# Kernel optimization log

Hardware: AMD Instinct MI355X
Metric: run time of the kernel (lower is better)

Reference implementation:

```python
import jax, jax.numpy as jnp
import numpy as np

N_NODES = 50000
N_EDGES = 1600000
IN_DIM = 128
HID = 64
EPS = 1e-6


def setup_inputs() -> dict:
    key = jax.random.key(0)
    ks = jax.random.split(key, 12)
    def g(k, shape, scale):
        return jax.random.normal(k, shape, dtype=jnp.float32) * scale
    x = g(ks[0], (N_NODES, IN_DIM), 1.0)
    edge_index = jax.random.randint(ks[1], (2, N_EDGES), 0, N_NODES, dtype=jnp.int64)
    return {
        "x": x,
        "edge_index": edge_index,
        "w0s": g(ks[2], (IN_DIM, HID), 1.0 / np.sqrt(IN_DIM)),
        "w0n": g(ks[3], (IN_DIM, HID), 1.0 / np.sqrt(IN_DIM)),
        "w1s": g(ks[4], (HID, HID), 1.0 / np.sqrt(HID)),
        "w1n": g(ks[5], (HID, HID), 1.0 / np.sqrt(HID)),
        "w2s": g(ks[6], (HID, HID), 1.0 / np.sqrt(HID)),
        "w2n": g(ks[7], (HID, HID), 1.0 / np.sqrt(HID)),
        "mw1": g(ks[8], (HID, 32), 1.0 / np.sqrt(HID)),
        "mb1": jnp.zeros((32,), jnp.float32),
        "mw2": g(ks[9], (32, 1), 1.0 / np.sqrt(32.0)),
        "mb2": jnp.zeros((1,), jnp.float32),
    }


def _uhg_layer(h, src, dst, inv_deg, ws, wn):
    # transform-then-gather (cheaper: GEMM at node granularity, gather at edge granularity)
    msg = (h @ wn)[src]                                    # [E, HID]
    agg = jax.ops.segment_sum(msg, dst, num_segments=N_NODES) * inv_deg  # mean over in-neighbors
    h2 = jax.nn.relu(h @ ws + agg)
    # projective (UHG) normalization: map embedding back onto the unit sphere / projective rep
    return h2 / (jnp.linalg.norm(h2, axis=-1, keepdims=True) + EPS)


def reference(x, edge_index, w0s, w0n, w1s, w1n, w2s, w2n, mw1, mb1, mw2, mb2):
    src, dst = edge_index[0], edge_index[1]
    deg = jax.ops.segment_sum(jnp.ones((N_EDGES,), jnp.float32), dst, num_segments=N_NODES)
    inv_deg = (1.0 / jnp.maximum(deg, 1.0))[:, None]       # [N,1]
    h = _uhg_layer(x, src, dst, inv_deg, w0s, w0n)
    h = _uhg_layer(h, src, dst, inv_deg, w1s, w1n)
    h = _uhg_layer(h, src, dst, inv_deg, w2s, w2n)
    h = jax.nn.relu(h @ mw1 + mb1)                         # [N,32]
    return jax.nn.sigmoid(h @ mw2 + mb2)                   # [N,1]
```

## Files before the change

### kernel.cpp

```cpp
#include <hip/hip_runtime.h>
#include <hip/hip_bf16.h>
#include <math.h>

#define N_NODES 50000
#define N_EDGES 1600000
#define IN_DIM  128
#define HID     64
#define EPB     4096
#define NBLK    391
#define NB      391
#define CAP     8192
#define PBKT    8192
#define GEMM0G  782
static constexpr float EPS = 1e-6f;

typedef __attribute__((ext_vector_type(8))) short          short8;
typedef __attribute__((ext_vector_type(4))) int            i32x4;
typedef __attribute__((ext_vector_type(4))) float          f32x4;
typedef __attribute__((ext_vector_type(2))) float          f32x2;

__device__ __forceinline__ unsigned short f2bf(float f) {
    union { float f; unsigned int i; } c; c.f = f;
    unsigned int r = c.i + 0x7FFFu + ((c.i >> 16) & 1u);
    return (unsigned short)(r >> 16);
}
__device__ __forceinline__ unsigned char f2fp8(float f) {
    int p = __builtin_amdgcn_cvt_pk_fp8_f32(f, f, 0, false);
    return (unsigned char)(p & 0xff);
}


template <int K>
__device__ __forceinline__ void pack_body(const float* __restrict__ wS,
                                          const float* __restrict__ wN,
                                          unsigned short* __restrict__ pS,
                                          unsigned short* __restrict__ pN, int blk) {
    constexpr int NSLOT = (K / 32) * 4 * 64;
    int slot = blk * 256 + (int)threadIdx.x;
    if (slot >= NSLOT) return;
    int lane = slot & 63;
    int ct   = slot >> 6;
    int t    = ct & 3;
    int c    = ct >> 2;
    int m    = lane & 15;
    int quad = lane >> 4;
    int col  = t * 16 + m;
#pragma unroll
    for (int j = 0; j < 8; ++j) {
        int k = c * 32 + quad * 8 + j;
        pS[slot * 8 + j] = f2bf(wS[k * 64 + col]);
        pN[slot * 8 + j] = f2bf(wN[k * 64 + col]);
    }
}

template <int K, bool F32IN>
__device__ __forceinline__ void gemm_body(
    const void* __restrict__ Av,
    const unsigned short* __restrict__ pS,
    const unsigned short* __restrict__ pN,
    float* __restrict__ hs, unsigned char* __restrict__ hnq, int blk) {
    constexpr int NC = K / 32;
    int lane = threadIdx.x & 63;
    int wv   = threadIdx.x >> 6;
    int tile = blk * 4 + wv;
    if (tile >= N_NODES / 16) return;
    int m    = lane & 15;
    int quad = lane >> 4;

    const short8* pSf = (const short8*)pS;
    const short8* pNf = (const short8*)pN;

    f32x4 accS[4], accN[4];
#pragma unroll
    for (int t = 0; t < 4; ++t) {
        accS[t] = (f32x4){0.f, 0.f, 0.f, 0.f};
        accN[t] = (f32x4){0.f, 0.f, 0.f, 0.f};
    }
#pragma unroll
    for (int c = 0; c < NC; ++c) {
        short8 a;
        if constexpr (F32IN) {
            const float* Af = (const float*)Av + ((size_t)tile * 16 + m) * K + quad * 8 + c * 32;
            f32x4 a0 = *(const f32x4*)Af;
            f32x4 a1 = *(const f32x4*)(Af + 4);
#pragma unroll
            for (int k = 0; k < 4; ++k) a[k]     = (short)f2bf(a0[k]);
#pragma unroll
            for (int k = 0; k < 4; ++k) a[k + 4] = (short)f2bf(a1[k]);
        } else {
            const short8* Af = (const short8*)((const unsigned short*)Av +
                               ((size_t)tile * 16 + m) * K + quad * 8);
            a = Af[c * 4];
        }
#pragma unroll
        for (int t = 0; t < 4; ++t) {
            short8 bs = pSf[(c * 4 + t) * 64 + lane];
            short8 bn = pNf[(c * 4 + t) * 64 + lane];
            accS[t] = __builtin_amdgcn_mfma_f32_16x16x32_bf16(a, bs, accS[t], 0, 0, 0);
            accN[t] = __builtin_amdgcn_mfma_f32_16x16x32_bf16(a, bn, accN[t], 0, 0, 0);
        }
    }
    int row0 = tile * 16 + quad * 4;
#pragma unroll
    for (int t = 0; t < 4; ++t) {
#pragma unroll
        for (int r = 0; r < 4; ++r) {
            size_t o = (size_t)(row0 + r) * HID + t * 16 + m;
            hs[o]  = accS[t][r];
            hnq[o] = f2fp8(accN[t][r]);
        }
    }
}

__global__ __launch_bounds__(256) void bucket_count_pack(
    const int* __restrict__ ei, int* __restrict__ bc,
    const float* __restrict__ w0s, const float* __restrict__ w0n,
    const float* __restrict__ w1s, const float* __restrict__ w1n,
    const float* __restrict__ w2s, const float* __restrict__ w2n,
    unsigned short* __restrict__ p0S, unsigned short* __restrict__ p0N,
    unsigned short* __restrict__ p1S, unsigned short* __restrict__ p1N,
    unsigned short* __restrict__ p2S, unsigned short* __restrict__ p2N,
    unsigned char* __restrict__ hnqA, unsigned char* __restrict__ hnqB,
    int* __restrict__ gcount) {
    if (blockIdx.x >= NBLK) {
        int blk = blockIdx.x - NBLK;
        if (blk == 7) {
            if (threadIdx.x >= 128 && threadIdx.x < 144)
                ((unsigned int*)(hnqA + (size_t)N_NODES * HID))[threadIdx.x - 128] = 0u;
            if (threadIdx.x >= 144 && threadIdx.x < 160)
                ((unsigned int*)(hnqB + (size_t)N_NODES * HID))[threadIdx.x - 144] = 0u;
            if (threadIdx.x == 160) gcount[0] = 0;
        }
        if (blk < 4)      pack_body<IN_DIM>(w0s, w0n, p0S, p0N, blk);
        else if (blk < 6) pack_body<HID>(w1s, w1n, p1S, p1N, blk - 4);
        else              pack_body<HID>(w2s, w2n, p2S, p2N, blk - 6);
        return;
    }
    __shared__ int hist[NB];
    for (int i = threadIdx.x; i < NB; i += 256) hist[i] = 0;
    __syncthreads();
    int base = blockIdx.x * EPB;
    int lim  = min(EPB, N_EDGES - base);
    for (int i = threadIdx.x; i < lim; i += 256)
        atomicAdd(&hist[ei[N_EDGES + base + i] >> 7], 1);
    __syncthreads();
    for (int b = threadIdx.x; b < NB; b += 256)
        bc[blockIdx.x * NB + b] = hist[b];
}

__global__ __launch_bounds__(256) void col_sumfix_gemm0(
    int* __restrict__ bc, int* __restrict__ bucketBase, int* __restrict__ bucketTot,
    int* __restrict__ gcount,
    const float* __restrict__ x,
    const unsigned short* __restrict__ p0S, const unsigned short* __restrict__ p0N,
    float* __restrict__ hs, unsigned char* __restrict__ hnq) {
    if (blockIdx.x >= NB) {
        gemm_body<IN_DIM, true>(x, p0S, p0N, hs, hnq, blockIdx.x - NB);
        return;
    }
    __shared__ int vals[NBLK];
    int b = blockIdx.x;
    for (int i = threadIdx.x; i < NBLK; i += 256) vals[i] = bc[i * NB + b];
    __syncthreads();
    if (threadIdx.x < 64) {
        int lane = threadIdx.x;
        int s = 0;
        for (int i = lane; i < NBLK; i += 64) s += vals[i];
#pragma unroll
        for (int off = 32; off >= 1; off >>= 1) s += __shfl_xor(s, off, 64);
        int base = 0;
        if (lane == 0) {
            base = atomicAdd(gcount, s);
            bucketBase[b] = base;
            bucketTot[b]  = s;
        }
        base = __shfl(base, 0, 64);
        int carry = base;
        for (int bs = 0; bs < NBLK; bs += 64) {
            int i = bs + lane;
            int v = (i < NBLK) ? vals[i] : 0;
            int incl = v;
#pragma unroll
            for (int off = 1; off < 64; off <<= 1) {
                int t = __shfl_up(incl, off, 64);
                if (lane >= off) incl += t;
            }
            if (i < NBLK) vals[i] = carry + incl - v;
            carry += __shfl(incl, 63, 64);
        }
    }
    __syncthreads();
    for (int i = threadIdx.x; i < NBLK; i += 256) bc[i * NB + b] = vals[i];
}

__global__ __launch_bounds__(256) void bucket_scatter(const int* __restrict__ ei,
                                                      const int* __restrict__ bc,
                                                      unsigned int* __restrict__ bucketPacked) {
    __shared__ int cur[NB];
    for (int b = threadIdx.x; b < NB; b += 256)
        cur[b] = bc[blockIdx.x * NB + b];
    __syncthreads();
    int base = blockIdx.x * EPB;
    int lim  = min(EPB, N_EDGES - base);
    for (int i = threadIdx.x; i < lim; i += 256) {
        int s = ei[base + i];
        int d = ei[N_EDGES + base + i];
        int pos = atomicAdd(&cur[d >> 7], 1);
        bucketPacked[pos] = ((unsigned int)s << 7) | (unsigned int)(d & 127);
    }
}

__global__ __launch_bounds__(256) void node_scan_scatter_pad(
    const unsigned int* __restrict__ bucketPacked,
    const int* __restrict__ bucketBase, const int* __restrict__ bucketTot,
    int* __restrict__ pbeg, int* __restrict__ rdeg, int* __restrict__ csr_pad) {
    __shared__ int cnt[128];
    __shared__ int half0;
    __shared__ unsigned int stage[CAP];
    int tid = threadIdx.x;
    if (tid < 128) cnt[tid] = 0;
    __syncthreads();
    int beg = bucketBase[blockIdx.x];
    int n   = bucketTot[blockIdx.x];
    for (int i = tid; i < n; i += 256) {
        unsigned int e = bucketPacked[beg + i];
        if (i < CAP) stage[i] = e;
        atomicAdd(&cnt[e & 127], 1);
    }
    __syncthreads();
    int lane = tid & 63;
    int v    = (tid < 128) ? cnt[tid] : 0;
    int vp   = (v + 7) & ~7;
    int incl = vp;
#pragma unroll
    for (int off = 1; off < 64; off <<= 1) {
        int t = __shfl_up(incl, off, 64);
        if (lane >= off) incl += t;
    }
    if (tid == 63) half0 = incl;
    __syncthreads();
    int start = blockIdx.x * PBKT + ((tid >= 64 && tid < 128) ? half0 : 0) + incl - vp;
    int node  = blockIdx.x * 128 + tid;
    if (tid < 128 && node < N_NODES) {
        pbeg[node] = start;
        rdeg[node] = v;
        for (int j = v; j < vp; ++j) csr_pad[start + j] = N_NODES;
        cnt[tid] = start;
    }
    __syncthreads();
    for (int i = tid; i < n; i += 256) {
        unsigned int e = (i < CAP) ? stage[i] : bucketPacked[beg + i];
        int pos = atomicAdd(&cnt[e & 127], 1);
        csr_pad[pos] = (int)(e >> 7);
    }
}

template <bool MLP>
__global__ __launch_bounds__(256) void agg_update(
    const int* __restrict__ pbeg, const int* __restrict__ rdeg,
    const int* __restrict__ csr_pad,
    const unsigned char* __restrict__ hnq, const float* __restrict__ hs,
    const unsigned short* __restrict__ pS, const unsigned short* __restrict__ pN,
    float* __restrict__ hs2, unsigned char* __restrict__ hnq2,
    const float* __restrict__ mw1, const float* __restrict__ mb1,
    const float* __restrict__ mw2, const float* __restrict__ mb2,
    float* __restrict__ out) {
    __shared__ unsigned short sA[MLP ? 1 : 16 * 80];
    __shared__ float sW1[MLP ? HID * 32 : 1];
    __shared__ float sW2[MLP ? 32 : 1];
    __shared__ float sB1[MLP ? 32 : 1];
    __shared__ float sH[MLP ? 16 * 68 : 1];
    if (MLP) {
        for (int i = threadIdx.x; i < HID * 32; i += 256) sW1[i] = mw1[i];
        if (threadIdx.x < 32) { sW2[threadIdx.x] = mw2[threadIdx.x]; sB1[threadIdx.x] = mb1[threadIdx.x]; }
        __syncthreads();
    }
    int sn   = threadIdx.x >> 4;
    int r    = threadIdx.x & 15;
    int node = blockIdx.x * 16 + sn;
    int beg  = pbeg[node];
    int dg   = rdeg[node];
    f32x4 h  = *(const f32x4*)(hs + (size_t)node * HID + r * 4);
    int nbat = (dg + 7) >> 3;
    const i32x4* ip = (const i32x4*)(csr_pad + beg);
    unsigned r4 = (unsigned)(r * 4);

    f32x2 acc2[2];
    acc2[0] = (f32x2){0.f, 0.f};
    acc2[1] = (f32x2){0.f, 0.f};

#pragma unroll 2
    for (int t = 0; t < nbat; ++t) {
        i32x4 a = ip[2 * t];
        i32x4 b = ip[2 * t + 1];
        unsigned wv[8];
#pragma unroll
        for (int u = 0; u < 4; ++u)
            wv[u]     = *(const unsigned*)(hnq + (((unsigned)a[u] << 6) + r4));
#pragma unroll
        for (int u = 0; u < 4; ++u)
            wv[u + 4] = *(const unsigned*)(hnq + (((unsigned)b[u] << 6) + r4));
#pragma unroll
        for (int u = 0; u < 8; ++u) {
#if __has_builtin(__builtin_amdgcn_cvt_pk_f32_fp8)
            acc2[0] += __builtin_amdgcn_cvt_pk_f32_fp8((int)wv[u], false);
            acc2[1] += __builtin_amdgcn_cvt_pk_f32_fp8((int)wv[u], true);
#else
            acc2[0] += (f32x2){__builtin_amdgcn_cvt_f32_fp8((int)wv[u], 0),
                               __builtin_amdgcn_cvt_f32_fp8((int)wv[u], 1)};
            acc2[1] += (f32x2){__builtin_amdgcn_cvt_f32_fp8((int)wv[u], 2),
                               __builtin_amdgcn_cvt_f32_fp8((int)wv[u], 3)};
#endif
        }
    }

    float acc[4] = {acc2[0][0], acc2[0][1], acc2[1][0], acc2[1][1]};
    float invdeg = 1.0f / fmaxf((float)dg, 1.0f);
    float v[4], ss = 0.f;
#pragma unroll
    for (int k = 0; k < 4; ++k) {
        v[k] = fmaxf(fmaf(acc[k], invdeg, h[k]), 0.f);
        ss += v[k] * v[k];
    }
    ss += __shfl_xor(ss, 1, 64);
    ss += __shfl_xor(ss, 2, 64);
    ss += __shfl_xor(ss, 4, 64);
    ss += __shfl_xor(ss, 8, 64);
    float rs = 1.0f / (sqrtf(ss) + EPS);

    if constexpr (!MLP) {
        unsigned short* ap = &sA[sn * 80 + r * 4];
#pragma unroll
        for (int k = 0; k < 4; ++k) ap[k] = f2bf(v[k] * rs);
        __syncthreads();
        int lane = threadIdx.x & 63;
        int wv_  = threadIdx.x >> 6;
        int m    = lane & 15;
        int quad = lane >> 4;
        const short8* pB = (const short8*)((wv_ < 2) ? pS : pN);
        int t0 = (wv_ & 1) * 2;
        f32x4 gacc[2];
        gacc[0] = (f32x4){0.f, 0.f, 0.f, 0.f};
        gacc[1] = (f32x4){0.f, 0.f, 0.f, 0.f};
#pragma unroll
        for (int c = 0; c < 2; ++c) {
            short8 a = *(const short8*)&sA[m * 80 + quad * 8 + c * 32];
#pragma unroll
            for (int tt = 0; tt < 2; ++tt) {
                short8 b = pB[(c * 4 + t0 + tt) * 64 + lane];
                gacc[tt] = __builtin_amdgcn_mfma_f32_16x16x32_bf16(a, b, gacc[tt], 0, 0, 0);
            }
        }
        int row0 = blockIdx.x * 16 + quad * 4;
#pragma unroll
        for (int tt = 0; tt < 2; ++tt) {
            int col = (t0 + tt) * 16 + m;
#pragma unroll
            for (int rr = 0; rr < 4; ++rr) {
                size_t o = (size_t)(row0 + rr) * HID + col;
                if (wv_ < 2) hs2[o]  = gacc[tt][rr];
                else         hnq2[o] = f2fp8(gacc[tt][rr]);
            }
        }
    } else {
#pragma unroll
        for (int k = 0; k < 4; ++k) sH[sn * 68 + r * 4 + k] = v[k] * rs;
        __syncthreads();
        int c0 = r * 2;
        float y0 = sB1[c0], y1 = sB1[c0 + 1];
        const float* hrow2 = &sH[sn * 68];
#pragma unroll 8
        for (int k = 0; k < HID; ++k) {
            float hv = hrow2[k];
            y0 = fmaf(hv, sW1[k * 32 + c0], y0);
            y1 = fmaf(hv, sW1[k * 32 + c0 + 1], y1);
        }
        float p = fmaxf(y0, 0.f) * sW2[c0] + fmaxf(y1, 0.f) * sW2[c0 + 1];
        p += __shfl_xor(p, 1, 64);
        p += __shfl_xor(p, 2, 64);
        p += __shfl_xor(p, 4, 64);
        p += __shfl_xor(p, 8, 64);
        if (r == 0) out[node] = 1.0f / (1.0f + __expf(-(p + mb2[0])));
    }
}

extern "C" void kernel_launch(void* const* d_in, const int* in_sizes, int n_in,
                              void* d_out, int out_size, void* d_ws, size_t ws_size,
                              hipStream_t stream) {
    const float* x   = (const float*)d_in[0];
    const int*   ei  = (const int*)d_in[1];
    const float* w0s = (const float*)d_in[2];
    const float* w0n = (const float*)d_in[3];
    const float* w1s = (const float*)d_in[4];
    const float* w1n = (const float*)d_in[5];
    const float* w2s = (const float*)d_in[6];
    const float* w2n = (const float*)d_in[7];
    const float* mw1 = (const float*)d_in[8];
    const float* mb1 = (const float*)d_in[9];
    const float* mw2 = (const float*)d_in[10];
    const float* mb2 = (const float*)d_in[11];
    float*       out = (float*)d_out;

    int* pbeg        = (int*)d_ws;
    int* rdeg        = pbeg + 50048;
    int* bc          = rdeg + 50048;
    int* bucketBase  = bc + 153600;
    int* bucketTot   = bucketBase + 512;
    int* gcount      = bucketTot + 512;
    unsigned int* bucketPacked = (unsigned int*)(gcount + 64);
    int* csr_pad     = (int*)(bucketPacked + N_EDGES);
    const size_t NH = (size_t)N_NODES * HID;
    float*          hsA  = (float*)(csr_pad + NB * PBKT);
    unsigned char*  hnqA = (unsigned char*)(hsA + NH);
    float*          hsB  = (float*)(hnqA + NH + 64);
    unsigned char*  hnqB = (unsigned char*)(hsB + NH);
    unsigned short* p0S = (unsigned short*)(hnqB + NH + 64);
    unsigned short* p0N = p0S + IN_DIM * HID;
    unsigned short* p1S = p0N + IN_DIM * HID;
    unsigned short* p1N = p1S + HID * HID;
    unsigned short* p2S = p1N + HID * HID;
    unsigned short* p2N = p2S + HID * HID;

    const int nodeGrid = N_NODES / 16;

    bucket_count_pack<<<NBLK + 8, 256, 0, stream>>>(
        ei, bc, w0s, w0n, w1s, w1n, w2s, w2n,
        p0S, p0N, p1S, p1N, p2S, p2N, hnqA, hnqB, gcount);
    col_sumfix_gemm0<<<NB + GEMM0G, 256, 0, stream>>>(
        bc, bucketBase, bucketTot, gcount, x, p0S, p0N, hsA, hnqA);
    bucket_scatter<<<NBLK, 256, 0, stream>>>(ei, bc, bucketPacked);
    node_scan_scatter_pad<<<NB, 256, 0, stream>>>(bucketPacked, bucketBase, bucketTot,
                                                  pbeg, rdeg, csr_pad);

    agg_update<false><<<nodeGrid, 256, 0, stream>>>(
        pbeg, rdeg, csr_pad, hnqA, hsA, p1S, p1N, hsB, hnqB,
        nullptr, nullptr, nullptr, nullptr, nullptr);

    agg_update<false><<<nodeGrid, 256, 0, stream>>>(
        pbeg, rdeg, csr_pad, hnqB, hsB, p2S, p2N, hsA, hnqA,
        nullptr, nullptr, nullptr, nullptr, nullptr);

    agg_update<true><<<nodeGrid, 256, 0, stream>>>(
        pbeg, rdeg, csr_pad, hnqA, hsA, nullptr, nullptr, nullptr, nullptr,
        mw1, mb1, mw2, mb2, out);
}
```

Measured before the change: 205.9 us.

## Stage per-block CSR indices in LDS and pre-shift indices to byte offsets

The CSR build now stores neighbor indices pre-multiplied by 64, so the gather skips a shift per edge. Each aggregation block cooperatively loads its 16 nodes' contiguous padded index range (up to 2048 entries) into shared memory. Per-node loops then read indices from LDS instead of issuing scattered global vector loads, with a global fallback when the range overflows. This adds a block-wide sync and about 8KB of LDS per block, which may reduce occupancy.

```diff
diff --git a/kernel.cpp b/kernel.cpp
--- a/kernel.cpp
+++ b/kernel.cpp
@@ -12,6 +12,7 @@
 #define CAP     8192
 #define PBKT    8192
 #define GEMM0G  782
+#define TSTAGE  2048
 static constexpr float EPS = 1e-6f;
 
 typedef __attribute__((ext_vector_type(8))) short          short8;
@@ -244,14 +245,14 @@
     if (tid < 128 && node < N_NODES) {
         pbeg[node] = start;
         rdeg[node] = v;
-        for (int j = v; j < vp; ++j) csr_pad[start + j] = N_NODES;
+        for (int j = v; j < vp; ++j) csr_pad[start + j] = N_NODES << 6;
         cnt[tid] = start;
     }
     __syncthreads();
     for (int i = tid; i < n; i += 256) {
         unsigned int e = (i < CAP) ? stage[i] : bucketPacked[beg + i];
         int pos = atomicAdd(&cnt[e & 127], 1);
-        csr_pad[pos] = (int)(e >> 7);
+        csr_pad[pos] = (int)((e >> 7) << 6);
     }
 }
 
@@ -265,6 +266,7 @@
     const float* __restrict__ mw1, const float* __restrict__ mb1,
     const float* __restrict__ mw2, const float* __restrict__ mb2,
     float* __restrict__ out) {
+    __shared__ int sIdx[TSTAGE];
     __shared__ unsigned short sA[MLP ? 1 : 16 * 80];
     __shared__ float sW1[MLP ? HID * 32 : 1];
     __shared__ float sW2[MLP ? 32 : 1];
@@ -273,46 +275,56 @@
     if (MLP) {
         for (int i = threadIdx.x; i < HID * 32; i += 256) sW1[i] = mw1[i];
         if (threadIdx.x < 32) { sW2[threadIdx.x] = mw2[threadIdx.x]; sB1[threadIdx.x] = mb1[threadIdx.x]; }
-        __syncthreads();
     }
     int sn   = threadIdx.x >> 4;
     int r    = threadIdx.x & 15;
     int node = blockIdx.x * 16 + sn;
+    int node0 = blockIdx.x * 16;
+    int tbeg  = pbeg[node0];
+    int tend  = pbeg[node0 + 15] + ((rdeg[node0 + 15] + 7) & ~7);
+    int nstage = min(tend - tbeg, TSTAGE);
+    for (int i = threadIdx.x; i < nstage; i += 256) sIdx[i] = csr_pad[tbeg + i];
+    __syncthreads();
+
     int beg  = pbeg[node];
     int dg   = rdeg[node];
     f32x4 h  = *(const f32x4*)(hs + (size_t)node * HID + r * 4);
     int nbat = (dg + 7) >> 3;
-    const i32x4* ip = (const i32x4*)(csr_pad + beg);
-    unsigned r4 = (unsigned)(r * 4);
+    int local = beg - tbeg;
+    bool useL = (local + nbat * 8) <= nstage;
+    const unsigned char* hnqr = hnq + r * 4;
 
     f32x2 acc2[2];
     acc2[0] = (f32x2){0.f, 0.f};
     acc2[1] = (f32x2){0.f, 0.f};
 
-#pragma unroll 2
-    for (int t = 0; t < nbat; ++t) {
-        i32x4 a = ip[2 * t];
-        i32x4 b = ip[2 * t + 1];
-        unsigned wv[8];
-#pragma unroll
-        for (int u = 0; u < 4; ++u)
-            wv[u]     = *(const unsigned*)(hnq + (((unsigned)a[u] << 6) + r4));
-#pragma unroll
-        for (int u = 0; u < 4; ++u)
-            wv[u + 4] = *(const unsigned*)(hnq + (((unsigned)b[u] << 6) + r4));
-#pragma unroll
-        for (int u = 0; u < 8; ++u) {
-#if __has_builtin(__builtin_amdgcn_cvt_pk_f32_fp8)
-            acc2[0] += __builtin_amdgcn_cvt_pk_f32_fp8((int)wv[u], false);
-            acc2[1] += __builtin_amdgcn_cvt_pk_f32_fp8((int)wv[u], true);
-#else
-            acc2[0] += (f32x2){__builtin_amdgcn_cvt_f32_fp8((int)wv[u], 0),
-                               __builtin_amdgcn_cvt_f32_fp8((int)wv[u], 1)};
-            acc2[1] += (f32x2){__builtin_amdgcn_cvt_f32_fp8((int)wv[u], 2),
-                               __builtin_amdgcn_cvt_f32_fp8((int)wv[u], 3)};
-#endif
-        }
-    }
+#define AGG_LOOP(IP)                                                          \
+    _Pragma("unroll 2")                                                       \
+    for (int t = 0; t < nbat; ++t) {                                          \
+        i32x4 a = (IP)[2 * t];                                                \
+        i32x4 b = (IP)[2 * t + 1];                                            \
+        unsigned wv[8];                                                       \
+        _Pragma("unroll")                                                     \
+        for (int u = 0; u < 4; ++u)                                           \
+            wv[u]     = *(const unsigned*)(hnqr + (unsigned)a[u]);            \
+        _Pragma("unroll")                                                     \
+        for (int u = 0; u < 4; ++u)                                           \
+            wv[u + 4] = *(const unsigned*)(hnqr + (unsigned)b[u]);            \
+        _Pragma("unroll")                                                     \
+        for (int u = 0; u < 8; ++u) {                                         \
+            acc2[0] += __builtin_amdgcn_cvt_pk_f32_fp8((int)wv[u], false);    \
+            acc2[1] += __builtin_amdgcn_cvt_pk_f32_fp8((int)wv[u], true);     \
+        }                                                                     \
+    }
+
+    if (useL) {
+        const i32x4* ipL = (const i32x4*)&sIdx[local];
+        AGG_LOOP(ipL)
+    } else {
+        const i32x4* ipG = (const i32x4*)(csr_pad + beg);
+        AGG_LOOP(ipG)
+    }
+#undef AGG_LOOP
 
     float acc[4] = {acc2[0][0], acc2[0][1], acc2[1][0], acc2[1][1]};
     float invdeg = 1.0f / fmaxf((float)dg, 1.0f);
```

New measurement: 210.1 us. 2.0% more time.
